# Performance work log

Hardware: AMD Instinct MI355X
Metric: run time of the kernel (lower is better)

The kernel has to match this reference:

```python
import jax, jax.numpy as jnp
import numpy as np
import math

E = 8          # num_experts
IN = 1024      # input_size
HID = 512      # head_size (expert hidden)
TOP_K = 2
B, P = 8, 1024


def setup_inputs() -> dict:
    key = jax.random.key(0)
    k1, k2, k3, k4, k5 = jax.random.split(key, 5)
    # expert weights init like ParallelExperts.reset_parameters (uniform xavier-ish)
    std1 = math.sqrt(2.0 / (IN + HID)); a1 = math.sqrt(3.0) * std1
    std2 = math.sqrt(2.0 / (HID + IN)); a2 = math.sqrt(3.0) * std2
    return {
        "x": jax.random.normal(k1, (B, P, IN), dtype=jnp.float32),
        "Q_isp": jax.random.normal(k2, (B, P, 1, IN), dtype=jnp.float32),
        "K_isp": jax.random.normal(k3, (B, P, E, IN), dtype=jnp.float32),
        "w1": jax.random.uniform(k4, (E, IN, HID), minval=-a1, maxval=a1, dtype=jnp.float32),
        "w2": jax.random.uniform(k5, (E, HID, IN), minval=-a2, maxval=a2, dtype=jnp.float32),
    }


def _gates(Q_isp, K_isp):
    # attention-based gating, eval path (no noise)
    N = K_isp.shape[2]
    scale = 1.0 / math.sqrt(K_isp.shape[-1])
    # [B,P,1,N] -> [T,N]
    scores = jnp.einsum('bpqd,bpnd->bpqn', Q_isp, K_isp)[:, :, 0, :].reshape(-1, N) * scale
    logits = jnp.nan_to_num(scores, nan=0.0, posinf=20.0, neginf=-20.0)
    probs = jax.nn.softmax(logits, axis=1)
    top_g, top_i = jax.lax.top_k(probs, TOP_K)
    # renormalize top-k gates; denominator detached as in torch (.detach())
    top_g = top_g / jax.lax.stop_gradient(top_g.sum(axis=1, keepdims=True) + 1e-6)
    T = probs.shape[0]
    gates = jnp.zeros_like(probs).at[jnp.arange(T)[:, None], top_i].set(top_g)
    return gates  # [T, E]


def reference(x, Q_isp, K_isp, w1, w2):
    gates = _gates(Q_isp, K_isp)                       # [T,E]
    T = gates.shape[0]
    xt = x.reshape(T, -1)                              # [T,IN]
    # grouped expert GEMMs (dense-masked form; gates are 0 off top-k)
    h = jax.nn.gelu(jnp.einsum('ti,eio->teo', xt, w1), approximate=False)  # [T,E,HID]
    y = jnp.einsum('teo,eoi->tei', h, w2)              # [T,E,IN]
    out = jnp.einsum('tei,te->ti', y, gates)           # combine with gates
    return out.reshape(x.shape)
```

## Files before the change

### kernel.cpp

```cpp
#include <hip/hip_runtime.h>
#include <math.h>

#define TT 8192
#define NE 8
#define DIN 1024
#define DH 512

typedef __attribute__((ext_vector_type(8))) short short8;
typedef __attribute__((ext_vector_type(4))) float f32x4;
typedef __attribute__((ext_vector_type(4))) unsigned short us4;

static const size_t OFF_CNT    = 0;
static const size_t OFF_BASE   = 256;
static const size_t OFF_TOKEXP = 512;
static const size_t OFF_GPAIR  = OFF_TOKEXP + (size_t)TT * 8;
static const size_t OFF_SLOT0  = OFF_GPAIR  + (size_t)TT * 8;
static const size_t OFF_SLOT1  = OFF_SLOT0  + (size_t)TT * 4;
static const size_t OFF_TOK    = OFF_SLOT1  + (size_t)TT * 4;
static const size_t OFF_GATE   = OFF_TOK    + (size_t)NE * TT * 4;
static const size_t OFF_XB     = OFF_GATE   + (size_t)NE * TT * 4;
static const size_t OFF_W1T    = OFF_XB     + (size_t)TT * DIN * 2;
static const size_t OFF_W2T    = OFF_W1T    + (size_t)NE * DH * DIN * 2;
static const size_t OFF_H      = OFF_W2T    + (size_t)NE * DIN * DH * 2;
static const size_t OFF_Y      = OFF_H      + (size_t)2 * TT * DH * 2;

__device__ __forceinline__ unsigned short f2bf(float f) {
    union { float f; unsigned u; } v; v.f = f;
    unsigned r = (v.u + 0x7fffu + ((v.u >> 16) & 1u)) >> 16;
    return (unsigned short)r;
}
__device__ __forceinline__ float bf2f(unsigned short u) {
    union { unsigned u; float f; } v; v.u = ((unsigned)u) << 16;
    return v.f;
}
__device__ __forceinline__ void async_copy16(const void* g, void* l) {
    __builtin_amdgcn_global_load_lds(
        (const __attribute__((address_space(1))) void*)g,
        (__attribute__((address_space(3))) void*)l, 16, 0, 0);
}

__device__ __forceinline__ float gelu_erf(float u) {
    float z  = 0.70710678118f * u;
    float az = fabsf(z);
    float t  = __builtin_amdgcn_rcpf(__builtin_fmaf(0.3275911f, az, 1.0f));
    float p  = t * (0.254829592f + t * (-0.284496736f + t * (1.421413741f +
               t * (-1.453152027f + t * 1.061405429f))));
    float e2 = exp2f(-1.4426950408889634f * az * az);
    float er = __builtin_fmaf(-p, e2, 1.0f);
    er = copysignf(er, z);
    return 0.5f * u * (1.0f + er);
}

__global__ __launch_bounds__(256) void prep_kernel(
    const float* __restrict__ x, const float* __restrict__ w1, const float* __restrict__ w2,
    const float* __restrict__ Q, const float* __restrict__ Kc,
    unsigned short* __restrict__ xb, unsigned short* __restrict__ w1t,
    unsigned short* __restrict__ w2t,
    int2* __restrict__ tokexp, float2* __restrict__ gpair)
{
    __shared__ float tile[32][33];
    int bid = blockIdx.x;
    int tid = threadIdx.x;

    if (bid < 4096) {
        size_t i = ((size_t)bid * 256 + tid) * 8;
        float4 a = *reinterpret_cast<const float4*>(x + i);
        float4 b = *reinterpret_cast<const float4*>(x + i + 4);
        us4 o0 = { f2bf(a.x), f2bf(a.y), f2bf(a.z), f2bf(a.w) };
        us4 o1 = { f2bf(b.x), f2bf(b.y), f2bf(b.z), f2bf(b.w) };
        *reinterpret_cast<us4*>(xb + i)     = o0;
        *reinterpret_cast<us4*>(xb + i + 4) = o1;
    } else if (bid < 12288) {
        const float* src; unsigned short* dst; int K, N, e, k0, n0;
        if (bid < 8192) {
            int r = bid - 4096; e = r >> 9; int rem = r & 511;
            k0 = (rem & 31) * 32; n0 = (rem >> 5) * 32;
            src = w1; dst = w1t; K = DIN; N = DH;
        } else {
            int r = bid - 8192; e = r >> 9; int rem = r & 511;
            k0 = (rem & 15) * 32; n0 = (rem >> 4) * 32;
            src = w2; dst = w2t; K = DH; N = DIN;
        }
        int tx = tid & 31, ty = tid >> 5;
        const float* s = src + ((size_t)e * K + k0) * N + n0;
#pragma unroll
        for (int r2 = 0; r2 < 32; r2 += 8) tile[ty + r2][tx] = s[(size_t)(ty + r2) * N + tx];
        __syncthreads();
        unsigned short* d = dst + ((size_t)e * N + n0) * K + k0;
#pragma unroll
        for (int r2 = 0; r2 < 32; r2 += 8) d[(size_t)(ty + r2) * K + tx] = f2bf(tile[tx][ty + r2]);
    } else {
        int wave = tid >> 6, lane = tid & 63;
        int t = (bid - 12288) * 4 + wave;
        const float4* q4 = reinterpret_cast<const float4*>(Q + (size_t)t * DIN);
        const float4* k4 = reinterpret_cast<const float4*>(Kc + (size_t)t * NE * DIN);
        float4 q[4];
#pragma unroll
        for (int j = 0; j < 4; ++j) q[j] = q4[j * 64 + lane];
        float part[NE];
#pragma unroll
        for (int e = 0; e < NE; ++e) {
            float s = 0.0f;
#pragma unroll
            for (int j = 0; j < 4; ++j) {
                float4 kv = k4[e * 256 + j * 64 + lane];
                s += q[j].x * kv.x + q[j].y * kv.y + q[j].z * kv.z + q[j].w * kv.w;
            }
            part[e] = s;
        }
#pragma unroll
        for (int e = 0; e < NE; ++e) {
#pragma unroll
            for (int m = 1; m < 64; m <<= 1) part[e] += __shfl_xor(part[e], m);
        }
        if (lane == 0) {
            float s[NE];
#pragma unroll
            for (int e = 0; e < NE; ++e) {
                float v = part[e] * 0.03125f;
                if (isnan(v)) v = 0.0f;
                else if (isinf(v)) v = (v > 0.0f) ? 20.0f : -20.0f;
                s[e] = v;
            }
            float m = s[0];
            for (int e = 1; e < NE; ++e) m = fmaxf(m, s[e]);
            float p[NE]; float sum = 0.0f;
            for (int e = 0; e < NE; ++e) { p[e] = expf(s[e] - m); sum += p[e]; }
            float inv = 1.0f / sum;
            for (int e = 0; e < NE; ++e) p[e] *= inv;
            int i0 = 0;
            for (int e = 1; e < NE; ++e) if (p[e] > p[i0]) i0 = e;
            int i1 = (i0 == 0) ? 1 : 0;
            for (int e = 0; e < NE; ++e) if (e != i0 && p[e] > p[i1]) i1 = e;
            float denom = p[i0] + p[i1] + 1e-6f;
            tokexp[t] = make_int2(i0, i1);
            gpair[t]  = make_float2(p[i0] / denom, p[i1] / denom);
        }
    }
}

__global__ __launch_bounds__(1024) void route_kernel(
    const int2* __restrict__ tokexp, const float2* __restrict__ gpair,
    int* __restrict__ cnt, int* __restrict__ base,
    int* __restrict__ tok_list, float* __restrict__ gate_list,
    int* __restrict__ slot0, int* __restrict__ slot1)
{
    int e = blockIdx.x;
    int tid = threadIdx.x;
    int wave = tid >> 6, lane = tid & 63;
    __shared__ int hist[NE];
    __shared__ int wsum[16];
    __shared__ int running;

    if (tid < NE) hist[tid] = 0;
    __syncthreads();

    int lc[NE];
#pragma unroll
    for (int j = 0; j < NE; ++j) lc[j] = 0;
#pragma unroll
    for (int r = 0; r < TT / 1024; ++r) {
        int2 te = tokexp[r * 1024 + tid];
#pragma unroll
        for (int j = 0; j < NE; ++j) lc[j] += (te.x == j ? 1 : 0) + (te.y == j ? 1 : 0);
    }
#pragma unroll
    for (int j = 0; j < NE; ++j) {
        int v = lc[j];
#pragma unroll
        for (int m = 1; m < 64; m <<= 1) v += __shfl_xor(v, m);
        if (lane == 0) atomicAdd(&hist[j], v);
    }
    __syncthreads();

    int b = 0;
#pragma unroll
    for (int j = 0; j < NE; ++j) if (j < e) b += hist[j];
    if (tid == 0) { cnt[e] = hist[e]; base[e] = b; running = b; }
    __syncthreads();

    int eb = b;
#pragma unroll 1
    for (int r = 0; r < TT / 1024; ++r) {
        int t = r * 1024 + tid;
        int2 te = tokexp[t];
        float2 g = gpair[t];
        bool f0 = (te.x == e), f1 = (te.y == e);
        bool f = f0 || f1;
        unsigned long long mask = __ballot(f);
        int mypos = __popcll(mask & ((1ull << lane) - 1ull));
        if (lane == 0) wsum[wave] = __popcll(mask);
        __syncthreads();
        int off = 0, total = 0;
        for (int w = 0; w < 16; ++w) {
            int c = wsum[w];
            if (w < wave) off += c;
            total += c;
        }
        int pos = running + off + mypos;
        if (f) {
            int j = pos - eb;
            tok_list[e * TT + j]  = t;
            gate_list[e * TT + j] = f0 ? g.x : g.y;
            if (f0) slot0[t] = pos; else slot1[t] = pos;
        }
        __syncthreads();
        if (tid == 0) running += total;
        __syncthreads();
    }
}

__global__ __launch_bounds__(256) void gemm1_kernel(
    const unsigned short* __restrict__ xb, const unsigned short* __restrict__ w1t,
    const int* __restrict__ cnt, const int* __restrict__ base,
    const int* __restrict__ tok_list, unsigned short* __restrict__ h)
{
    int e = blockIdx.z;
    int Te = cnt[e];
    int m0 = blockIdx.x * 128;
    if (m0 >= Te) return;
    int n0 = blockIdx.y * 128;

    __shared__ __align__(16) char smem[65536];

    int tid = threadIdx.x;
    int w = tid >> 6, lane = tid & 63;
    int wm = w & 1, wn = w >> 1;
    int mcol = lane & 15;
    int kq = (lane >> 4) * 8;

    int ia0 = m0 + (2 * w + 0) * 16 + mcol;
    int ia1 = m0 + (2 * w + 1) * 16 + mcol;
    int ra0 = (ia0 < Te) ? tok_list[e * TT + ia0] : 0;
    int ra1 = (ia1 < Te) ? tok_list[e * TT + ia1] : 0;

    const unsigned short* w1e = w1t + (size_t)e * DH * DIN;
    const unsigned short* pa0 = xb + (size_t)ra0 * DIN + kq;
    const unsigned short* pa1 = xb + (size_t)ra1 * DIN + kq;
    const unsigned short* pb0 = w1e + (size_t)(n0 + (2 * w + 0) * 16 + mcol) * DIN + kq;
    const unsigned short* pb1 = w1e + (size_t)(n0 + (2 * w + 1) * 16 + mcol) * DIN + kq;

    int d0 = (2 * w + 0) * 1024;
    int d1 = (2 * w + 1) * 1024;

#define STAGE1(buf, koff) do { \
    async_copy16(pa0 + (koff),      (buf) + d0); \
    async_copy16(pa1 + (koff),      (buf) + d1); \
    async_copy16(pa0 + (koff) + 32, (buf) + 8192  + d0); \
    async_copy16(pa1 + (koff) + 32, (buf) + 8192  + d1); \
    async_copy16(pb0 + (koff),      (buf) + 16384 + d0); \
    async_copy16(pb1 + (koff),      (buf) + 16384 + d1); \
    async_copy16(pb0 + (koff) + 32, (buf) + 24576 + d0); \
    async_copy16(pb1 + (koff) + 32, (buf) + 24576 + d1); \
} while (0)

    f32x4 acc[4][4];
#pragma unroll
    for (int i = 0; i < 4; i++)
#pragma unroll
        for (int j = 0; j < 4; j++) acc[i][j] = {0.f, 0.f, 0.f, 0.f};

    char* cur = smem;
    char* nxt = smem + 32768;

    STAGE1(cur, 0);
    __syncthreads();

    const int NT = DIN / 64;
    for (int t = 0; t < NT; ++t) {
        if (t + 1 < NT) STAGE1(nxt, (t + 1) * 64);
#pragma unroll
        for (int half = 0; half < 2; ++half) {
            const char* cb = cur + half * 8192;
            short8 af[4], bfr[4];
#pragma unroll
            for (int mt = 0; mt < 4; ++mt)
                af[mt] = *reinterpret_cast<const short8*>(cb + (wm * 4 + mt) * 1024 + lane * 16);
#pragma unroll
            for (int nt = 0; nt < 4; ++nt)
                bfr[nt] = *reinterpret_cast<const short8*>(cb + 16384 + (wn * 4 + nt) * 1024 + lane * 16);
#pragma unroll
            for (int mt = 0; mt < 4; ++mt)
#pragma unroll
                for (int nt = 0; nt < 4; ++nt)
                    acc[mt][nt] = __builtin_amdgcn_mfma_f32_16x16x32_bf16(af[mt], bfr[nt], acc[mt][nt], 0, 0, 0);
        }
        __syncthreads();
        char* tmp = cur; cur = nxt; nxt = tmp;
    }
#undef STAGE1

    int hb = base[e] + m0;
#pragma unroll
    for (int mt = 0; mt < 4; ++mt) {
        int rbase = (wm * 4 + mt) * 16 + ((lane >> 4) * 4);
#pragma unroll
        for (int r = 0; r < 4; ++r) {
            int row = rbase + r;
            if (m0 + row < Te) {
#pragma unroll
                for (int nt = 0; nt < 4; ++nt) {
                    float g = gelu_erf(acc[mt][nt][r]);
                    int col = n0 + (wn * 4 + nt) * 16 + mcol;
                    h[(size_t)(hb + row) * DH + col] = f2bf(g);
                }
            }
        }
    }
}

__global__ __launch_bounds__(256) void gemm2_kernel(
    const unsigned short* __restrict__ h, const unsigned short* __restrict__ w2t,
    const int* __restrict__ cnt, const int* __restrict__ base,
    const float* __restrict__ gate_list, unsigned short* __restrict__ y)
{
    int e = blockIdx.z;
    int Te = cnt[e];
    int m0 = blockIdx.x * 128;
    if (m0 >= Te) return;
    int n0 = blockIdx.y * 128;

    __shared__ __align__(16) char smem[65536];

    int tid = threadIdx.x;
    int w = tid >> 6, lane = tid & 63;
    int wm = w & 1, wn = w >> 1;
    int mcol = lane & 15;
    int kq = (lane >> 4) * 8;
    int hb = base[e];

    int r0 = m0 + (2 * w + 0) * 16 + mcol; if (r0 >= Te) r0 = Te - 1;
    int r1 = m0 + (2 * w + 1) * 16 + mcol; if (r1 >= Te) r1 = Te - 1;
    const unsigned short* w2e = w2t + (size_t)e * DIN * DH;
    const unsigned short* pa0 = h + (size_t)(hb + r0) * DH + kq;
    const unsigned short* pa1 = h + (size_t)(hb + r1) * DH + kq;
    const unsigned short* pb0 = w2e + (size_t)(n0 + (2 * w + 0) * 16 + mcol) * DH + kq;
    const unsigned short* pb1 = w2e + (size_t)(n0 + (2 * w + 1) * 16 + mcol) * DH + kq;

    int d0 = (2 * w + 0) * 1024;
    int d1 = (2 * w + 1) * 1024;

#define STAGE2(buf, koff) do { \
    async_copy16(pa0 + (koff),      (buf) + d0); \
    async_copy16(pa1 + (koff),      (buf) + d1); \
    async_copy16(pa0 + (koff) + 32, (buf) + 8192  + d0); \
    async_copy16(pa1 + (koff) + 32, (buf) + 8192  + d1); \
    async_copy16(pb0 + (koff),      (buf) + 16384 + d0); \
    async_copy16(pb1 + (koff),      (buf) + 16384 + d1); \
    async_copy16(pb0 + (koff) + 32, (buf) + 24576 + d0); \
    async_copy16(pb1 + (koff) + 32, (buf) + 24576 + d1); \
} while (0)

    f32x4 acc[4][4];
#pragma unroll
    for (int i = 0; i < 4; i++)
#pragma unroll
        for (int j = 0; j < 4; j++) acc[i][j] = {0.f, 0.f, 0.f, 0.f};

    char* cur = smem;
    char* nxt = smem + 32768;

    STAGE2(cur, 0);
    __syncthreads();

    const int NT = DH / 64;
    for (int t = 0; t < NT; ++t) {
        if (t + 1 < NT) STAGE2(nxt, (t + 1) * 64);
#pragma unroll
        for (int half = 0; half < 2; ++half) {
            const char* cb = cur + half * 8192;
            short8 af[4], bfr[4];
#pragma unroll
            for (int mt = 0; mt < 4; ++mt)
                af[mt] = *reinterpret_cast<const short8*>(cb + (wm * 4 + mt) * 1024 + lane * 16);
#pragma unroll
            for (int nt = 0; nt < 4; ++nt)
                bfr[nt] = *reinterpret_cast<const short8*>(cb + 16384 + (wn * 4 + nt) * 1024 + lane * 16);
#pragma unroll
            for (int mt = 0; mt < 4; ++mt)
#pragma unroll
                for (int nt = 0; nt < 4; ++nt)
                    acc[mt][nt] = __builtin_amdgcn_mfma_f32_16x16x32_bf16(af[mt], bfr[nt], acc[mt][nt], 0, 0, 0);
        }
        __syncthreads();
        char* tmp = cur; cur = nxt; nxt = tmp;
    }
#undef STAGE2

#pragma unroll
    for (int mt = 0; mt < 4; ++mt) {
        int rbase = (wm * 4 + mt) * 16 + ((lane >> 4) * 4);
#pragma unroll
        for (int r = 0; r < 4; ++r) {
            int row = rbase + r;
            if (m0 + row < Te) {
                float g = gate_list[e * TT + m0 + row];
#pragma unroll
                for (int nt = 0; nt < 4; ++nt) {
                    int col = n0 + (wn * 4 + nt) * 16 + mcol;
                    y[(size_t)(hb + m0 + row) * DIN + col] = f2bf(acc[mt][nt][r] * g);
                }
            }
        }
    }
}

__global__ __launch_bounds__(256) void combine_kernel(
    const unsigned short* __restrict__ y,
    const int* __restrict__ slot0, const int* __restrict__ slot1,
    float* __restrict__ out)
{
    int c = threadIdx.x * 4;
#pragma unroll
    for (int r = 0; r < 4; ++r) {
        int t = blockIdx.x * 4 + r;
        const unsigned short* y0 = y + (size_t)slot0[t] * DIN + c;
        const unsigned short* y1 = y + (size_t)slot1[t] * DIN + c;
        us4 u0 = *reinterpret_cast<const us4*>(y0);
        us4 u1 = *reinterpret_cast<const us4*>(y1);
        float4 o;
        o.x = bf2f(u0.x) + bf2f(u1.x);
        o.y = bf2f(u0.y) + bf2f(u1.y);
        o.z = bf2f(u0.z) + bf2f(u1.z);
        o.w = bf2f(u0.w) + bf2f(u1.w);
        *reinterpret_cast<float4*>(out + (size_t)t * DIN + c) = o;
    }
}

extern "C" void kernel_launch(void* const* d_in, const int* in_sizes, int n_in,
                              void* d_out, int out_size, void* d_ws, size_t ws_size,
                              hipStream_t stream) {
    const float* x  = (const float*)d_in[0];
    const float* Q  = (const float*)d_in[1];
    const float* K  = (const float*)d_in[2];
    const float* w1 = (const float*)d_in[3];
    const float* w2 = (const float*)d_in[4];
    float* out = (float*)d_out;

    char* ws = (char*)d_ws;
    int*    cnt       = (int*)(ws + OFF_CNT);
    int*    base      = (int*)(ws + OFF_BASE);
    int2*   tokexp    = (int2*)(ws + OFF_TOKEXP);
    float2* gpair     = (float2*)(ws + OFF_GPAIR);
    int*    slot0     = (int*)(ws + OFF_SLOT0);
    int*    slot1     = (int*)(ws + OFF_SLOT1);
    int*    tok_list  = (int*)(ws + OFF_TOK);
    float*  gate_list = (float*)(ws + OFF_GATE);
    unsigned short* xb  = (unsigned short*)(ws + OFF_XB);
    unsigned short* w1t = (unsigned short*)(ws + OFF_W1T);
    unsigned short* w2t = (unsigned short*)(ws + OFF_W2T);
    unsigned short* h   = (unsigned short*)(ws + OFF_H);
    unsigned short* y   = (unsigned short*)(ws + OFF_Y);

    prep_kernel<<<14336, 256, 0, stream>>>(x, w1, w2, Q, K, xb, w1t, w2t, tokexp, gpair);
    route_kernel<<<NE, 1024, 0, stream>>>(tokexp, gpair, cnt, base,
                                          tok_list, gate_list, slot0, slot1);
    gemm1_kernel<<<dim3(TT / 128, DH / 128, NE), 256, 0, stream>>>(xb, w1t, cnt, base, tok_list, h);
    gemm2_kernel<<<dim3(TT / 128, DIN / 128, NE), 256, 0, stream>>>(h, w2t, cnt, base, gate_list, y);
    combine_kernel<<<TT / 4, 256, 0, stream>>>(y, slot0, slot1, out);
}
```

Measured before the change: 610.1 us.

## Pad expert segments to tiles, flatten grid, fuse combine into gemm2 via atomics

Each expert's token segment is padded to a multiple of 128 so the GEMM grids run over a flat list of tiles (MT_MAX by N) instead of a 3D grid with many early-exit blocks. The combine kernel and the bf16 y buffer are removed: gemm2 scales by the gate and atomically adds fp32 results straight into the output, which prep_kernel now zeroes. Routing also drops the slot arrays. This removes a kernel launch and the y round-trip to memory, at the cost of fp32 atomic traffic on the output and extra work on padded rows.

```diff
diff --git a/kernel.cpp b/kernel.cpp
--- a/kernel.cpp
+++ b/kernel.cpp
@@ -5,33 +5,26 @@
 #define NE 8
 #define DIN 1024
 #define DH 512
+#define MT_MAX 136
 
 typedef __attribute__((ext_vector_type(8))) short short8;
 typedef __attribute__((ext_vector_type(4))) float f32x4;
 typedef __attribute__((ext_vector_type(4))) unsigned short us4;
 
-static const size_t OFF_CNT    = 0;
-static const size_t OFF_BASE   = 256;
-static const size_t OFF_TOKEXP = 512;
+static const size_t OFF_BASE   = 0;
+static const size_t OFF_TOKEXP = 256;
 static const size_t OFF_GPAIR  = OFF_TOKEXP + (size_t)TT * 8;
-static const size_t OFF_SLOT0  = OFF_GPAIR  + (size_t)TT * 8;
-static const size_t OFF_SLOT1  = OFF_SLOT0  + (size_t)TT * 4;
-static const size_t OFF_TOK    = OFF_SLOT1  + (size_t)TT * 4;
-static const size_t OFF_GATE   = OFF_TOK    + (size_t)NE * TT * 4;
-static const size_t OFF_XB     = OFF_GATE   + (size_t)NE * TT * 4;
+static const size_t OFF_TOK    = OFF_GPAIR  + (size_t)TT * 8;
+static const size_t OFF_GATE   = OFF_TOK    + (size_t)(2 * TT + NE * 128) * 4;
+static const size_t OFF_XB     = OFF_GATE   + (size_t)(2 * TT + NE * 128) * 4;
 static const size_t OFF_W1T    = OFF_XB     + (size_t)TT * DIN * 2;
 static const size_t OFF_W2T    = OFF_W1T    + (size_t)NE * DH * DIN * 2;
 static const size_t OFF_H      = OFF_W2T    + (size_t)NE * DIN * DH * 2;
-static const size_t OFF_Y      = OFF_H      + (size_t)2 * TT * DH * 2;
 
 __device__ __forceinline__ unsigned short f2bf(float f) {
     union { float f; unsigned u; } v; v.f = f;
     unsigned r = (v.u + 0x7fffu + ((v.u >> 16) & 1u)) >> 16;
     return (unsigned short)r;
-}
-__device__ __forceinline__ float bf2f(unsigned short u) {
-    union { unsigned u; float f; } v; v.u = ((unsigned)u) << 16;
-    return v.f;
 }
 __device__ __forceinline__ void async_copy16(const void* g, void* l) {
     __builtin_amdgcn_global_load_lds(
@@ -56,42 +49,16 @@
     const float* __restrict__ Q, const float* __restrict__ Kc,
     unsigned short* __restrict__ xb, unsigned short* __restrict__ w1t,
     unsigned short* __restrict__ w2t,
-    int2* __restrict__ tokexp, float2* __restrict__ gpair)
+    int2* __restrict__ tokexp, float2* __restrict__ gpair,
+    float* __restrict__ out)
 {
     __shared__ float tile[32][33];
     int bid = blockIdx.x;
     int tid = threadIdx.x;
 
-    if (bid < 4096) {
-        size_t i = ((size_t)bid * 256 + tid) * 8;
-        float4 a = *reinterpret_cast<const float4*>(x + i);
-        float4 b = *reinterpret_cast<const float4*>(x + i + 4);
-        us4 o0 = { f2bf(a.x), f2bf(a.y), f2bf(a.z), f2bf(a.w) };
-        us4 o1 = { f2bf(b.x), f2bf(b.y), f2bf(b.z), f2bf(b.w) };
-        *reinterpret_cast<us4*>(xb + i)     = o0;
-        *reinterpret_cast<us4*>(xb + i + 4) = o1;
-    } else if (bid < 12288) {
-        const float* src; unsigned short* dst; int K, N, e, k0, n0;
-        if (bid < 8192) {
-            int r = bid - 4096; e = r >> 9; int rem = r & 511;
-            k0 = (rem & 31) * 32; n0 = (rem >> 5) * 32;
-            src = w1; dst = w1t; K = DIN; N = DH;
-        } else {
-            int r = bid - 8192; e = r >> 9; int rem = r & 511;
-            k0 = (rem & 15) * 32; n0 = (rem >> 4) * 32;
-            src = w2; dst = w2t; K = DH; N = DIN;
-        }
-        int tx = tid & 31, ty = tid >> 5;
-        const float* s = src + ((size_t)e * K + k0) * N + n0;
-#pragma unroll
-        for (int r2 = 0; r2 < 32; r2 += 8) tile[ty + r2][tx] = s[(size_t)(ty + r2) * N + tx];
-        __syncthreads();
-        unsigned short* d = dst + ((size_t)e * N + n0) * K + k0;
-#pragma unroll
-        for (int r2 = 0; r2 < 32; r2 += 8) d[(size_t)(ty + r2) * K + tx] = f2bf(tile[tx][ty + r2]);
-    } else {
+    if (bid < 2048) {
         int wave = tid >> 6, lane = tid & 63;
-        int t = (bid - 12288) * 4 + wave;
+        int t = bid * 4 + wave;
         const float4* q4 = reinterpret_cast<const float4*>(Q + (size_t)t * DIN);
         const float4* k4 = reinterpret_cast<const float4*>(Kc + (size_t)t * NE * DIN);
         float4 q[4];
@@ -136,14 +103,46 @@
             tokexp[t] = make_int2(i0, i1);
             gpair[t]  = make_float2(p[i0] / denom, p[i1] / denom);
         }
+    } else if (bid < 4096) {
+        size_t i = ((size_t)(bid - 2048) * 256 + tid) * 16;
+        float4 z = {0.f, 0.f, 0.f, 0.f};
+#pragma unroll
+        for (int j = 0; j < 4; ++j)
+            *reinterpret_cast<float4*>(out + i + j * 4) = z;
+    } else if (bid < 8192) {
+        size_t i = ((size_t)(bid - 4096) * 256 + tid) * 8;
+        float4 a = *reinterpret_cast<const float4*>(x + i);
+        float4 b = *reinterpret_cast<const float4*>(x + i + 4);
+        us4 o0 = { f2bf(a.x), f2bf(a.y), f2bf(a.z), f2bf(a.w) };
+        us4 o1 = { f2bf(b.x), f2bf(b.y), f2bf(b.z), f2bf(b.w) };
+        *reinterpret_cast<us4*>(xb + i)     = o0;
+        *reinterpret_cast<us4*>(xb + i + 4) = o1;
+    } else {
+        const float* src; unsigned short* dst; int K, N, e, k0, n0;
+        if (bid < 12288) {
+            int r = bid - 8192; e = r >> 9; int rem = r & 511;
+            k0 = (rem & 31) * 32; n0 = (rem >> 5) * 32;
+            src = w1; dst = w1t; K = DIN; N = DH;
+        } else {
+            int r = bid - 12288; e = r >> 9; int rem = r & 511;
+            k0 = (rem & 15) * 32; n0 = (rem >> 4) * 32;
+            src = w2; dst = w2t; K = DH; N = DIN;
+        }
+        int tx = tid & 31, ty = tid >> 5;
+        const float* s = src + ((size_t)e * K + k0) * N + n0;
+#pragma unroll
+        for (int r2 = 0; r2 < 32; r2 += 8) tile[ty + r2][tx] = s[(size_t)(ty + r2) * N + tx];
+        __syncthreads();
+        unsigned short* d = dst + ((size_t)e * N + n0) * K + k0;
+#pragma unroll
+        for (int r2 = 0; r2 < 32; r2 += 8) d[(size_t)(ty + r2) * K + tx] = f2bf(tile[tx][ty + r2]);
     }
 }
 
 __global__ __launch_bounds__(1024) void route_kernel(
     const int2* __restrict__ tokexp, const float2* __restrict__ gpair,
-    int* __restrict__ cnt, int* __restrict__ base,
-    int* __restrict__ tok_list, float* __restrict__ gate_list,
-    int* __restrict__ slot0, int* __restrict__ slot1)
+    int* __restrict__ base,
+    int* __restrict__ tok_list, float* __restrict__ gate_list)
 {
     int e = blockIdx.x;
     int tid = threadIdx.x;
@@ -173,13 +172,20 @@
     }
     __syncthreads();
 
-    int b = 0;
-#pragma unroll
-    for (int j = 0; j < NE; ++j) if (j < e) b += hist[j];
-    if (tid == 0) { cnt[e] = hist[e]; base[e] = b; running = b; }
+    int basep[NE + 1];
+    basep[0] = 0;
+#pragma unroll
+    for (int j = 0; j < NE; ++j) basep[j + 1] = basep[j] + ((hist[j] + 127) & ~127);
+
+    if (tid == 0) {
+        base[e] = basep[e];
+        if (e == 0) base[NE] = basep[NE];
+        running = basep[e];
+    }
     __syncthreads();
 
-    int eb = b;
+    int myb = basep[e];
+    int cnt_e = hist[e];
 #pragma unroll 1
     for (int r = 0; r < TT / 1024; ++r) {
         int t = r * 1024 + tid;
@@ -199,26 +205,35 @@
         }
         int pos = running + off + mypos;
         if (f) {
-            int j = pos - eb;
-            tok_list[e * TT + j]  = t;
-            gate_list[e * TT + j] = f0 ? g.x : g.y;
-            if (f0) slot0[t] = pos; else slot1[t] = pos;
+            tok_list[pos]  = t;
+            gate_list[pos] = f0 ? g.x : g.y;
         }
         __syncthreads();
         if (tid == 0) running += total;
         __syncthreads();
+    }
+
+    int padn = ((cnt_e + 127) & ~127) - cnt_e;
+    if (tid < padn) {
+        tok_list[myb + cnt_e + tid]  = 0;
+        gate_list[myb + cnt_e + tid] = 0.0f;
     }
 }
 
 __global__ __launch_bounds__(256) void gemm1_kernel(
     const unsigned short* __restrict__ xb, const unsigned short* __restrict__ w1t,
-    const int* __restrict__ cnt, const int* __restrict__ base,
+    const int* __restrict__ base,
     const int* __restrict__ tok_list, unsigned short* __restrict__ h)
 {
-    int e = blockIdx.z;
-    int Te = cnt[e];
-    int m0 = blockIdx.x * 128;
-    if (m0 >= Te) return;
+    int bv[NE + 1];
+#pragma unroll
+    for (int i = 0; i <= NE; ++i) bv[i] = base[i];
+    int g0 = blockIdx.x * 128;
+    if (g0 >= bv[NE]) return;
+    int e = 0;
+#pragma unroll
+    for (int i = 1; i < NE; ++i) if (g0 >= bv[i]) e = i;
+
     int n0 = blockIdx.y * 128;
 
     __shared__ __align__(16) char smem[65536];
@@ -229,10 +244,8 @@
     int mcol = lane & 15;
     int kq = (lane >> 4) * 8;
 
-    int ia0 = m0 + (2 * w + 0) * 16 + mcol;
-    int ia1 = m0 + (2 * w + 1) * 16 + mcol;
-    int ra0 = (ia0 < Te) ? tok_list[e * TT + ia0] : 0;
-    int ra1 = (ia1 < Te) ? tok_list[e * TT + ia1] : 0;
+    int ra0 = tok_list[g0 + (2 * w + 0) * 16 + mcol];
+    int ra1 = tok_list[g0 + (2 * w + 1) * 16 + mcol];
 
     const unsigned short* w1e = w1t + (size_t)e * DH * DIN;
     const unsigned short* pa0 = xb + (size_t)ra0 * DIN + kq;
@@ -290,20 +303,17 @@
     }
 #undef STAGE1
 
-    int hb = base[e] + m0;
 #pragma unroll
     for (int mt = 0; mt < 4; ++mt) {
         int rbase = (wm * 4 + mt) * 16 + ((lane >> 4) * 4);
 #pragma unroll
         for (int r = 0; r < 4; ++r) {
             int row = rbase + r;
-            if (m0 + row < Te) {
-#pragma unroll
-                for (int nt = 0; nt < 4; ++nt) {
-                    float g = gelu_erf(acc[mt][nt][r]);
-                    int col = n0 + (wn * 4 + nt) * 16 + mcol;
-                    h[(size_t)(hb + row) * DH + col] = f2bf(g);
-                }
+#pragma unroll
+            for (int nt = 0; nt < 4; ++nt) {
+                float g = gelu_erf(acc[mt][nt][r]);
+                int col = n0 + (wn * 4 + nt) * 16 + mcol;
+                h[(size_t)(g0 + row) * DH + col] = f2bf(g);
             }
         }
     }
@@ -311,13 +321,19 @@
 
 __global__ __launch_bounds__(256) void gemm2_kernel(
     const unsigned short* __restrict__ h, const unsigned short* __restrict__ w2t,
-    const int* __restrict__ cnt, const int* __restrict__ base,
-    const float* __restrict__ gate_list, unsigned short* __restrict__ y)
+    const int* __restrict__ base,
+    const int* __restrict__ tok_list, const float* __restrict__ gate_list,
+    float* __restrict__ out)
 {
-    int e = blockIdx.z;
-    int Te = cnt[e];
-    int m0 = blockIdx.x * 128;
-    if (m0 >= Te) return;
+    int bv[NE + 1];
+#pragma unroll
+    for (int i = 0; i <= NE; ++i) bv[i] = base[i];
+    int g0 = blockIdx.x * 128;
+    if (g0 >= bv[NE]) return;
+    int e = 0;
+#pragma unroll
+    for (int i = 1; i < NE; ++i) if (g0 >= bv[i]) e = i;
+
     int n0 = blockIdx.y * 128;
 
     __shared__ __align__(16) char smem[65536];
@@ -327,13 +343,10 @@
     int wm = w & 1, wn = w >> 1;
     int mcol = lane & 15;
     int kq = (lane >> 4) * 8;
-    int hb = base[e];
-
-    int r0 = m0 + (2 * w + 0) * 16 + mcol; if (r0 >= Te) r0 = Te - 1;
-    int r1 = m0 + (2 * w + 1) * 16 + mcol; if (r1 >= Te) r1 = Te - 1;
+
     const unsigned short* w2e = w2t + (size_t)e * DIN * DH;
-    const unsigned short* pa0 = h + (size_t)(hb + r0) * DH + kq;
-    const unsigned short* pa1 = h + (size_t)(hb + r1) * DH + kq;
+    const unsigned short* pa0 = h + (size_t)(g0 + (2 * w + 0) * 16 + mcol) * DH + kq;
+    const unsigned short* pa1 = h + (size_t)(g0 + (2 * w + 1) * 16 + mcol) * DH + kq;
     const unsigned short* pb0 = w2e + (size_t)(n0 + (2 * w + 0) * 16 + mcol) * DH + kq;
     const unsigned short* pb1 = w2e + (size_t)(n0 + (2 * w + 1) * 16 + mcol) * DH + kq;
 
@@ -393,37 +406,14 @@
 #pragma unroll
         for (int r = 0; r < 4; ++r) {
             int row = rbase + r;
-            if (m0 + row < Te) {
-                float g = gate_list[e * TT + m0 + row];
-#pragma unroll
-                for (int nt = 0; nt < 4; ++nt) {
-                    int col = n0 + (wn * 4 + nt) * 16 + mcol;
-                    y[(size_t)(hb + m0 + row) * DIN + col] = f2bf(acc[mt][nt][r] * g);
-                }
+            int tok = tok_list[g0 + row];
+            float g = gate_list[g0 + row];
+#pragma unroll
+            for (int nt = 0; nt < 4; ++nt) {
+                int col = n0 + (wn * 4 + nt) * 16 + mcol;
+                atomicAdd(&out[(size_t)tok * DIN + col], acc[mt][nt][r] * g);
             }
         }
-    }
-}
-
-__global__ __launch_bounds__(256) void combine_kernel(
-    const unsigned short* __restrict__ y,
-    const int* __restrict__ slot0, const int* __restrict__ slot1,
-    float* __restrict__ out)
-{
-    int c = threadIdx.x * 4;
-#pragma unroll
-    for (int r = 0; r < 4; ++r) {
-        int t = blockIdx.x * 4 + r;
-        const unsigned short* y0 = y + (size_t)slot0[t] * DIN + c;
-        const unsigned short* y1 = y + (size_t)slot1[t] * DIN + c;
-        us4 u0 = *reinterpret_cast<const us4*>(y0);
-        us4 u1 = *reinterpret_cast<const us4*>(y1);
-        float4 o;
-        o.x = bf2f(u0.x) + bf2f(u1.x);
-        o.y = bf2f(u0.y) + bf2f(u1.y);
-        o.z = bf2f(u0.z) + bf2f(u1.z);
-        o.w = bf2f(u0.w) + bf2f(u1.w);
-        *reinterpret_cast<float4*>(out + (size_t)t * DIN + c) = o;
     }
 }
 
@@ -438,24 +428,18 @@
     float* out = (float*)d_out;
 
     char* ws = (char*)d_ws;
-    int*    cnt       = (int*)(ws + OFF_CNT);
     int*    base      = (int*)(ws + OFF_BASE);
     int2*   tokexp    = (int2*)(ws + OFF_TOKEXP);
     float2* gpair     = (float2*)(ws + OFF_GPAIR);
-    int*    slot0     = (int*)(ws + OFF_SLOT0);
-    int*    slot1     = (int*)(ws + OFF_SLOT1);
     int*    tok_list  = (int*)(ws + OFF_TOK);
     float*  gate_list = (float*)(ws + OFF_GATE);
     unsigned short* xb  = (unsigned short*)(ws + OFF_XB);
     unsigned short* w1t = (unsigned short*)(ws + OFF_W1T);
     unsigned short* w2t = (unsigned short*)(ws + OFF_W2T);
     unsigned short* h   = (unsigned short*)(ws + OFF_H);
-    unsigned short* y   = (unsigned short*)(ws + OFF_Y);
-
-    prep_kernel<<<14336, 256, 0, stream>>>(x, w1, w2, Q, K, xb, w1t, w2t, tokexp, gpair);
-    route_kernel<<<NE, 1024, 0, stream>>>(tokexp, gpair, cnt, base,
-                                          tok_list, gate_list, slot0, slot1);
-    gemm1_kernel<<<dim3(TT / 128, DH / 128, NE), 256, 0, stream>>>(xb, w1t, cnt, base, tok_list, h);
-    gemm2_kernel<<<dim3(TT / 128, DIN / 128, NE), 256, 0, stream>>>(h, w2t, cnt, base, gate_list, y);
-    combine_kernel<<<TT / 4, 256, 0, stream>>>(y, slot0, slot1, out);
-}
+
+    prep_kernel<<<16384, 256, 0, stream>>>(x, w1, w2, Q, K, xb, w1t, w2t, tokexp, gpair, out);
+    route_kernel<<<NE, 1024, 0, stream>>>(tokexp, gpair, base, tok_list, gate_list);
+    gemm1_kernel<<<dim3(MT_MAX, DH / 128), 256, 0, stream>>>(xb, w1t, base, tok_list, h);
+    gemm2_kernel<<<dim3(MT_MAX, DIN / 128), 256, 0, stream>>>(h, w2t, base, tok_list, gate_list, out);
+}
```

New measurement: 655.7 us. 1.07x slower.
